# Kernel optimization log

Hardware: AMD Instinct MI355X
Metric: run time of the kernel (lower is better)

## Reference

```python
import jax, jax.numpy as jnp
import numpy as np

B, T, I, H = 1024, 2048, 12, 512


def setup_inputs() -> dict:
    key = jax.random.key(0)
    k1, k2, k3, k4 = jax.random.split(key, 4)
    s = 1.0 / np.sqrt(H)
    return {
        "history": jax.random.normal(k1, (B, T, I), dtype=jnp.float32),
        "w_ih": jax.random.normal(k2, (3 * H, I), dtype=jnp.float32) * s,
        "w_hh": jax.random.normal(k3, (3 * H, H), dtype=jnp.float32) * s,
        "w_out": jax.random.normal(k4, (2, H), dtype=jnp.float32) * s,
        "b_out": jnp.zeros((2,), dtype=jnp.float32),
    }


def reference(history, w_ih, w_hh, w_out, b_out):
    # GRUCell recurrence over T steps with per-step linear head (torch GRUCell math, bias=False)
    xs = jnp.transpose(history, (1, 0, 2))  # [T, B, I]
    h0 = jnp.zeros((history.shape[0], H), dtype=history.dtype)

    def step(h, x_t):
        gi = x_t @ w_ih.T            # [B, 3H]
        gh = h @ w_hh.T              # [B, 3H]
        i_r, i_z, i_n = jnp.split(gi, 3, axis=-1)
        h_r, h_z, h_n = jnp.split(gh, 3, axis=-1)
        r = jax.nn.sigmoid(i_r + h_r)
        z = jax.nn.sigmoid(i_z + h_z)
        n = jnp.tanh(i_n + r * h_n)
        h_new = (1.0 - z) * n + z * h
        logit = h_new @ w_out.T + b_out  # [B, 2]
        return h_new, logit

    h_final, logits = jax.lax.scan(step, h0, xs)
    return jnp.transpose(logits, (1, 0, 2)), h_final  # ([B, T, 2], [B, H])
```

## Files before the change

### kernel.cpp

```cpp
#include <hip/hip_runtime.h>
#include <stdint.h>


#define NB 256
#define NT 256
#define TB 1024
#define TT 2048
#define II 12
#define HH 512
#define NCL 32
#define ROWS 32

#define HTILE_B (ROWS * HH * 2)
#define HBUF_B  ((size_t)NCL * HTILE_B)
#define BAR_OFF ((size_t)2 * HBUF_B)
#define WS_USED (BAR_OFF + (size_t)NCL * 256)

#define LDSB (ROWS * 1024)

#define GAS __attribute__((address_space(1)))
#define LAS __attribute__((address_space(3)))

typedef _Float16 half8 __attribute__((ext_vector_type(8)));
typedef float    f32x4 __attribute__((ext_vector_type(4)));

static __device__ __forceinline__ float fast_sigmoid(float x) {
  float e = exp2f(-1.44269504f * x);
  return __builtin_amdgcn_rcpf(1.0f + e);
}
static __device__ __forceinline__ float fast_tanh(float x) {
  float e = exp2f(2.88539008f * x);
  return 1.0f - 2.0f * __builtin_amdgcn_rcpf(1.0f + e);
}

static __device__ __forceinline__ void wait_flags32(unsigned* f, unsigned tgt,
                                                    int* dead) {
  const int l = threadIdx.x & 63;
  long spin = 0;
  for (;;) {
    unsigned v = __hip_atomic_load(f + (l & 31), __ATOMIC_RELAXED,
                                   __HIP_MEMORY_SCOPE_AGENT);
    if (__all(v >= tgt)) break;
    if (++spin > (1L << 24)) { *dead = 1; break; }
  }
}

__global__ void __launch_bounds__(NT, 1)
gru_persistent(const float* __restrict__ hist,
               const float* __restrict__ w_ih,
               const float* __restrict__ w_hh,
               const float* __restrict__ w_out,
               const float* __restrict__ b_out,
               float* __restrict__ out,
               uint8_t* __restrict__ ws)
{
  extern __shared__ char smem[];
  char* ldsA = smem;
  const int bid = blockIdx.x;
  const int c   = bid & 31;
  const int g   = bid >> 5;
  const int tid = threadIdx.x;
  const int w   = tid >> 6;
  const int l   = tid & 63;
  const int l15 = l & 15;
  const int l4  = l >> 4;
  const int crb = c * ROWS;
  unsigned* loF = (unsigned*)(ws + BAR_OFF) + (size_t)c * 64;
  unsigned* hiF = loF + 32;
  const int myflag = g * 4 + w;

  const int col0 = g * 64 + w * 16;
  const int pcol = col0 + l15;

  half8 wr[16], wz[16], wn[16];
#pragma unroll
  for (int ks = 0; ks < 16; ++ks) {
    const size_t Rr = (size_t)(0 * HH + col0 + l15) * HH + ks * 32 + l4 * 8;
    const size_t Rz = (size_t)(1 * HH + col0 + l15) * HH + ks * 32 + l4 * 8;
    const size_t Rn = (size_t)(2 * HH + col0 + l15) * HH + ks * 32 + l4 * 8;
#pragma unroll
    for (int i = 0; i < 8; ++i) {
      wr[ks][i] = (_Float16)w_hh[Rr + i];
      wz[ks][i] = (_Float16)w_hh[Rz + i];
      wn[ks][i] = (_Float16)w_hh[Rn + i];
    }
  }

  half8 wih[3];
#pragma unroll
  for (int gt = 0; gt < 3; ++gt) {
    const int R = gt * HH + col0 + l15;
#pragma unroll
    for (int i = 0; i < 8; ++i) {
      const int k = l4 * 8 + i;
      wih[gt][i] = (_Float16)((k < II) ? w_ih[R * II + k] : 0.0f);
    }
  }

  const int jj   = myflag & 1;
  const int erow = myflag >> 1;
  float wor8[8];
#pragma unroll
  for (int i = 0; i < 8; ++i) wor8[i] = w_out[jj * HH + l * 8 + i];
  const float bo = b_out[jj];

  float hprev[2][4];
#pragma unroll
  for (int mt = 0; mt < 2; ++mt)
#pragma unroll
    for (int q = 0; q < 4; ++q) hprev[mt][q] = 0.0f;

  int deadlock = 0;

  f32x4 xn0[2], xn1[2];
#pragma unroll
  for (int mt = 0; mt < 2; ++mt) {
    xn0[mt] = (f32x4){0.f, 0.f, 0.f, 0.f};
    xn1[mt] = (f32x4){0.f, 0.f, 0.f, 0.f};
    const float* xp = hist + (size_t)(crb + mt * 16 + l15) * (TT * II);
    if (l4 == 0)      { xn0[mt] = *(const f32x4*)xp; xn1[mt] = *(const f32x4*)(xp + 4); }
    else if (l4 == 1) { xn0[mt] = *(const f32x4*)(xp + 8); }
  }
  asm volatile("s_waitcnt vmcnt(0)" ::: "memory");

  unsigned preLo = 0, preHi = 0;

  for (int t = 0; t < TT; ++t) {
    const uint8_t* hsrc = ws + ((t & 1) ? HBUF_B : 0) + (size_t)c * HTILE_B;
    uint8_t*       hdst = ws + ((t & 1) ? 0 : HBUF_B) + (size_t)c * HTILE_B;

    if (t > 0) {
      if (!__all(preLo >= (unsigned)t)) wait_flags32(loF, (unsigned)t, &deadlock);
    }
    __builtin_amdgcn_sched_barrier(0);

#pragma unroll
    for (int it = 0; it < 4; ++it)
      __builtin_amdgcn_global_load_lds(
          (const GAS uint32_t*)(hsrc + it * 4096 + tid * 16),
          (LAS uint32_t*)(ldsA + it * 4096 + tid * 16), 16, 0, 17);
    __builtin_amdgcn_sched_barrier(0);

    preHi = __hip_atomic_load(hiF + (l & 31), __ATOMIC_RELAXED,
                              __HIP_MEMORY_SCOPE_AGENT);
    __builtin_amdgcn_sched_barrier(0);
    half8 ax[2];
#pragma unroll
    for (int mt = 0; mt < 2; ++mt)
#pragma unroll
      for (int i = 0; i < 4; ++i) {
        ax[mt][i]     = (_Float16)xn0[mt][i];
        ax[mt][4 + i] = (_Float16)xn1[mt][i];
      }
    {
      const int tx = (t + 1 < TT) ? (t + 1) : 0;
#pragma unroll
      for (int mt = 0; mt < 2; ++mt) {
        const float* xp = hist + (size_t)(crb + mt * 16 + l15) * (TT * II) + (size_t)tx * II;
        if (l4 == 0)      { xn0[mt] = *(const f32x4*)xp; xn1[mt] = *(const f32x4*)(xp + 4); }
        else if (l4 == 1) { xn0[mt] = *(const f32x4*)(xp + 8); }
      }
    }
    __builtin_amdgcn_sched_barrier(0);

    asm volatile("s_waitcnt vmcnt(6)" ::: "memory");
    __builtin_amdgcn_sched_barrier(0);
    if (t > 0 && !__all(preHi >= (unsigned)t)) wait_flags32(hiF, (unsigned)t, &deadlock);
    __builtin_amdgcn_sched_barrier(0);

#pragma unroll
    for (int it = 0; it < 4; ++it)
      __builtin_amdgcn_global_load_lds(
          (const GAS uint32_t*)(hsrc + 16384 + it * 4096 + tid * 16),
          (LAS uint32_t*)(ldsA + 16384 + it * 4096 + tid * 16), 16, 0, 17);
    __builtin_amdgcn_sched_barrier(0);

    __builtin_amdgcn_s_barrier();
    __builtin_amdgcn_sched_barrier(0);

    f32x4 acc0 = (f32x4){0.f, 0.f, 0.f, 0.f};
    f32x4 acc1 = acc0, acc2 = acc0;
    f32x4 accin = __builtin_amdgcn_mfma_f32_16x16x32_f16(ax[0], wih[2],
                    (f32x4){0.f, 0.f, 0.f, 0.f}, 0, 0, 0);
    acc0 = __builtin_amdgcn_mfma_f32_16x16x32_f16(ax[0], wih[0], acc0, 0, 0, 0);
    acc1 = __builtin_amdgcn_mfma_f32_16x16x32_f16(ax[0], wih[1], acc1, 0, 0, 0);
#pragma unroll
    for (int ks = 0; ks < 16; ++ks) {
      const int ko = (ks * 64 + l4 * 16) ^ ((l15 & 7) << 4);
      half8 a = *(const half8*)(ldsA + l15 * 1024 + ko);
      acc0 = __builtin_amdgcn_mfma_f32_16x16x32_f16(a, wr[ks], acc0, 0, 0, 0);
      acc1 = __builtin_amdgcn_mfma_f32_16x16x32_f16(a, wz[ks], acc1, 0, 0, 0);
      acc2 = __builtin_amdgcn_mfma_f32_16x16x32_f16(a, wn[ks], acc2, 0, 0, 0);
    }

#pragma unroll
    for (int q = 0; q < 4; ++q) {
      const int m = l4 * 4 + q;
      const float r  = fast_sigmoid(acc0[q]);
      const float z  = fast_sigmoid(acc1[q]);
      const float n  = fast_tanh(accin[q] + r * acc2[q]);
      const float hn = (1.0f - z) * n + z * hprev[0][q];
      hprev[0][q] = hn;
      __hip_atomic_store(
          (unsigned short*)(hdst + m * 1024 + ((pcol * 2) ^ ((m & 7) << 4))),
          __builtin_bit_cast(unsigned short, (_Float16)hn),
          __ATOMIC_RELAXED, __HIP_MEMORY_SCOPE_AGENT);
    }

    if (t > 0) {
      float s = 0.0f;
      half8 hv = *(const half8*)(ldsA + erow * 1024 + ((l * 16) ^ ((erow & 7) << 4)));
#pragma unroll
      for (int i = 0; i < 8; ++i) s += (float)hv[i] * wor8[i];
#pragma unroll
      for (int off = 1; off < 64; off <<= 1) s += __shfl_xor(s, off);
      if (l == 0) out[((size_t)(crb + erow) * TT + (t - 1)) * 2 + jj] = s + bo;
    }
    __builtin_amdgcn_sched_barrier(0);

    asm volatile("s_waitcnt vmcnt(0)" ::: "memory");
    __builtin_amdgcn_sched_barrier(0);
    if (l == 0)
      __hip_atomic_store(loF + myflag, (unsigned)(t + 1), __ATOMIC_RELAXED,
                         __HIP_MEMORY_SCOPE_AGENT);

    __builtin_amdgcn_s_barrier();
    __builtin_amdgcn_sched_barrier(0);

    acc0 = (f32x4){0.f, 0.f, 0.f, 0.f};
    acc1 = acc0; acc2 = acc0;
    accin = __builtin_amdgcn_mfma_f32_16x16x32_f16(ax[1], wih[2],
              (f32x4){0.f, 0.f, 0.f, 0.f}, 0, 0, 0);
    acc0 = __builtin_amdgcn_mfma_f32_16x16x32_f16(ax[1], wih[0], acc0, 0, 0, 0);
    acc1 = __builtin_amdgcn_mfma_f32_16x16x32_f16(ax[1], wih[1], acc1, 0, 0, 0);
#pragma unroll
    for (int ks = 0; ks < 16; ++ks) {
      const int ko = (ks * 64 + l4 * 16) ^ ((l15 & 7) << 4);
      half8 a = *(const half8*)(ldsA + (16 + l15) * 1024 + ko);
      acc0 = __builtin_amdgcn_mfma_f32_16x16x32_f16(a, wr[ks], acc0, 0, 0, 0);
      acc1 = __builtin_amdgcn_mfma_f32_16x16x32_f16(a, wz[ks], acc1, 0, 0, 0);
      acc2 = __builtin_amdgcn_mfma_f32_16x16x32_f16(a, wn[ks], acc2, 0, 0, 0);
    }
#pragma unroll
    for (int q = 0; q < 4; ++q) {
      const int m = 16 + l4 * 4 + q;
      const float r  = fast_sigmoid(acc0[q]);
      const float z  = fast_sigmoid(acc1[q]);
      const float n  = fast_tanh(accin[q] + r * acc2[q]);
      const float hn = (1.0f - z) * n + z * hprev[1][q];
      hprev[1][q] = hn;
      __hip_atomic_store(
          (unsigned short*)(hdst + m * 1024 + ((pcol * 2) ^ ((m & 7) << 4))),
          __builtin_bit_cast(unsigned short, (_Float16)hn),
          __ATOMIC_RELAXED, __HIP_MEMORY_SCOPE_AGENT);
    }

    if (t > 0) {
      const int lrw = 16 + erow;
      float s = 0.0f;
      half8 hv = *(const half8*)(ldsA + lrw * 1024 + ((l * 16) ^ ((lrw & 7) << 4)));
#pragma unroll
      for (int i = 0; i < 8; ++i) s += (float)hv[i] * wor8[i];
#pragma unroll
      for (int off = 1; off < 64; off <<= 1) s += __shfl_xor(s, off);
      if (l == 0) out[((size_t)(crb + lrw) * TT + (t - 1)) * 2 + jj] = s + bo;
    }
    __builtin_amdgcn_sched_barrier(0);

    asm volatile("s_waitcnt vmcnt(0)" ::: "memory");
    __builtin_amdgcn_sched_barrier(0);
    if (l == 0)
      __hip_atomic_store(hiF + myflag, (unsigned)(t + 1), __ATOMIC_RELAXED,
                         __HIP_MEMORY_SCOPE_AGENT);
    preLo = __hip_atomic_load(loF + (l & 31), __ATOMIC_RELAXED,
                              __HIP_MEMORY_SCOPE_AGENT);
  }

  asm volatile("s_waitcnt vmcnt(0)" ::: "memory");
  wait_flags32(loF, (unsigned)TT, &deadlock);
  wait_flags32(hiF, (unsigned)TT, &deadlock);
  {
    const uint8_t* hsrc = ws + ((TT & 1) ? HBUF_B : 0) + (size_t)c * HTILE_B;
#pragma unroll
    for (int it = 0; it < 8; ++it)
      __builtin_amdgcn_global_load_lds(
          (const GAS uint32_t*)(hsrc + it * 4096 + tid * 16),
          (LAS uint32_t*)(ldsA + it * 4096 + tid * 16), 16, 0, 17);
    asm volatile("s_waitcnt vmcnt(0)" ::: "memory");
    __builtin_amdgcn_s_barrier();

#pragma unroll
    for (int half = 0; half < 2; ++half) {
      const int lrw = half * 16 + erow;
      float s = 0.0f;
      half8 hv = *(const half8*)(ldsA + lrw * 1024 + ((l * 16) ^ ((lrw & 7) << 4)));
#pragma unroll
      for (int i = 0; i < 8; ++i) s += (float)hv[i] * wor8[i];
#pragma unroll
      for (int off = 1; off < 64; off <<= 1) s += __shfl_xor(s, off);
      if (l == 0) out[((size_t)(crb + lrw) * TT + (TT - 1)) * 2 + jj] = s + bo;
    }
  }

#pragma unroll
  for (int mt = 0; mt < 2; ++mt)
#pragma unroll
    for (int q = 0; q < 4; ++q) {
      const int m = mt * 16 + l4 * 4 + q;
      out[(size_t)TB * TT * 2 + (size_t)(crb + m) * HH + pcol] = hprev[mt][q];
    }
}

extern "C" void kernel_launch(void* const* d_in, const int* in_sizes, int n_in,
                              void* d_out, int out_size, void* d_ws, size_t ws_size,
                              hipStream_t stream) {
  (void)in_sizes; (void)n_in; (void)out_size;
  if (ws_size < WS_USED) return;

  const float* hist  = (const float*)d_in[0];
  const float* w_ih  = (const float*)d_in[1];
  const float* w_hh  = (const float*)d_in[2];
  const float* w_out = (const float*)d_in[3];
  const float* b_out = (const float*)d_in[4];
  float* out = (float*)d_out;
  uint8_t* ws = (uint8_t*)d_ws;

  hipMemsetAsync(d_ws, 0, WS_USED, stream);

  void* args[] = {(void*)&hist, (void*)&w_ih, (void*)&w_hh, (void*)&w_out,
                  (void*)&b_out, (void*)&out, (void*)&ws};
  hipError_t e = hipLaunchCooperativeKernel((const void*)gru_persistent,
                                            dim3(NB), dim3(NT), args,
                                            (unsigned)LDSB, stream);
  if (e != hipSuccess) {
    gru_persistent<<<dim3(NB), dim3(NT), LDSB, stream>>>(
        hist, w_ih, w_hh, w_out, b_out, out, ws);
  }
}
```

Measured before the change: 9.109 ms.

## Merge split lo/hi step flags into one flag set and load full tile

```diff
diff --git a/kernel.cpp b/kernel.cpp
--- a/kernel.cpp
+++ b/kernel.cpp
@@ -14,7 +14,7 @@
 #define HTILE_B (ROWS * HH * 2)
 #define HBUF_B  ((size_t)NCL * HTILE_B)
 #define BAR_OFF ((size_t)2 * HBUF_B)
-#define WS_USED (BAR_OFF + (size_t)NCL * 256)
+#define WS_USED (BAR_OFF + (size_t)NCL * 128)
 
 #define LDSB (ROWS * 1024)
 
@@ -65,8 +65,7 @@
   const int l15 = l & 15;
   const int l4  = l >> 4;
   const int crb = c * ROWS;
-  unsigned* loF = (unsigned*)(ws + BAR_OFF) + (size_t)c * 64;
-  unsigned* hiF = loF + 32;
+  unsigned* F = (unsigned*)(ws + BAR_OFF) + (size_t)c * 32;
   const int myflag = g * 4 + w;
 
   const int col0 = g * 64 + w * 16;
@@ -121,29 +120,25 @@
     if (l4 == 0)      { xn0[mt] = *(const f32x4*)xp; xn1[mt] = *(const f32x4*)(xp + 4); }
     else if (l4 == 1) { xn0[mt] = *(const f32x4*)(xp + 8); }
   }
-  asm volatile("s_waitcnt vmcnt(0)" ::: "memory");
-
-  unsigned preLo = 0, preHi = 0;
+
+  unsigned preF = 0;
 
   for (int t = 0; t < TT; ++t) {
     const uint8_t* hsrc = ws + ((t & 1) ? HBUF_B : 0) + (size_t)c * HTILE_B;
     uint8_t*       hdst = ws + ((t & 1) ? 0 : HBUF_B) + (size_t)c * HTILE_B;
 
     if (t > 0) {
-      if (!__all(preLo >= (unsigned)t)) wait_flags32(loF, (unsigned)t, &deadlock);
-    }
-    __builtin_amdgcn_sched_barrier(0);
-
-#pragma unroll
-    for (int it = 0; it < 4; ++it)
+      if (!__all(preF >= (unsigned)t)) wait_flags32(F, (unsigned)t, &deadlock);
+    }
+    __builtin_amdgcn_sched_barrier(0);
+
+#pragma unroll
+    for (int it = 0; it < 8; ++it)
       __builtin_amdgcn_global_load_lds(
           (const GAS uint32_t*)(hsrc + it * 4096 + tid * 16),
           (LAS uint32_t*)(ldsA + it * 4096 + tid * 16), 16, 0, 17);
     __builtin_amdgcn_sched_barrier(0);
 
-    preHi = __hip_atomic_load(hiF + (l & 31), __ATOMIC_RELAXED,
-                              __HIP_MEMORY_SCOPE_AGENT);
-    __builtin_amdgcn_sched_barrier(0);
     half8 ax[2];
 #pragma unroll
     for (int mt = 0; mt < 2; ++mt)
@@ -152,29 +147,9 @@
         ax[mt][i]     = (_Float16)xn0[mt][i];
         ax[mt][4 + i] = (_Float16)xn1[mt][i];
       }
-    {
-      const int tx = (t + 1 < TT) ? (t + 1) : 0;
-#pragma unroll
-      for (int mt = 0; mt < 2; ++mt) {
-        const float* xp = hist + (size_t)(crb + mt * 16 + l15) * (TT * II) + (size_t)tx * II;
-        if (l4 == 0)      { xn0[mt] = *(const f32x4*)xp; xn1[mt] = *(const f32x4*)(xp + 4); }
-        else if (l4 == 1) { xn0[mt] = *(const f32x4*)(xp + 8); }
-      }
-    }
-    __builtin_amdgcn_sched_barrier(0);
-
-    asm volatile("s_waitcnt vmcnt(6)" ::: "memory");
-    __builtin_amdgcn_sched_barrier(0);
-    if (t > 0 && !__all(preHi >= (unsigned)t)) wait_flags32(hiF, (unsigned)t, &deadlock);
-    __builtin_amdgcn_sched_barrier(0);
-
-#pragma unroll
-    for (int it = 0; it < 4; ++it)
-      __builtin_amdgcn_global_load_lds(
-          (const GAS uint32_t*)(hsrc + 16384 + it * 4096 + tid * 16),
-          (LAS uint32_t*)(ldsA + 16384 + it * 4096 + tid * 16), 16, 0, 17);
-    __builtin_amdgcn_sched_barrier(0);
-
+    __builtin_amdgcn_sched_barrier(0);
+
+    asm volatile("s_waitcnt vmcnt(4)" ::: "memory");
     __builtin_amdgcn_s_barrier();
     __builtin_amdgcn_sched_barrier(0);
 
@@ -206,24 +181,9 @@
           __builtin_bit_cast(unsigned short, (_Float16)hn),
           __ATOMIC_RELAXED, __HIP_MEMORY_SCOPE_AGENT);
     }
-
-    if (t > 0) {
-      float s = 0.0f;
-      half8 hv = *(const half8*)(ldsA + erow * 1024 + ((l * 16) ^ ((erow & 7) << 4)));
-#pragma unroll
-      for (int i = 0; i < 8; ++i) s += (float)hv[i] * wor8[i];
-#pragma unroll
-      for (int off = 1; off < 64; off <<= 1) s += __shfl_xor(s, off);
-      if (l == 0) out[((size_t)(crb + erow) * TT + (t - 1)) * 2 + jj] = s + bo;
-    }
-    __builtin_amdgcn_sched_barrier(0);
-
-    asm volatile("s_waitcnt vmcnt(0)" ::: "memory");
-    __builtin_amdgcn_sched_barrier(0);
-    if (l == 0)
-      __hip_atomic_store(loF + myflag, (unsigned)(t + 1), __ATOMIC_RELAXED,
-                         __HIP_MEMORY_SCOPE_AGENT);
-
+    __builtin_amdgcn_sched_barrier(0);
+
+    asm volatile("s_waitcnt vmcnt(4)" ::: "memory");
     __builtin_amdgcn_s_barrier();
     __builtin_amdgcn_sched_barrier(0);
 
@@ -256,29 +216,42 @@
     }
 
     if (t > 0) {
-      const int lrw = 16 + erow;
-      float s = 0.0f;
-      half8 hv = *(const half8*)(ldsA + lrw * 1024 + ((l * 16) ^ ((lrw & 7) << 4)));
-#pragma unroll
-      for (int i = 0; i < 8; ++i) s += (float)hv[i] * wor8[i];
-#pragma unroll
-      for (int off = 1; off < 64; off <<= 1) s += __shfl_xor(s, off);
-      if (l == 0) out[((size_t)(crb + lrw) * TT + (t - 1)) * 2 + jj] = s + bo;
+#pragma unroll
+      for (int half = 0; half < 2; ++half) {
+        const int lrw = half * 16 + erow;
+        float s = 0.0f;
+        half8 hv = *(const half8*)(ldsA + lrw * 1024 + ((l * 16) ^ ((lrw & 7) << 4)));
+#pragma unroll
+        for (int i = 0; i < 8; ++i) s += (float)hv[i] * wor8[i];
+#pragma unroll
+        for (int off = 1; off < 64; off <<= 1) s += __shfl_xor(s, off);
+        if (l == 0) out[((size_t)(crb + lrw) * TT + (t - 1)) * 2 + jj] = s + bo;
+      }
     }
     __builtin_amdgcn_sched_barrier(0);
 
     asm volatile("s_waitcnt vmcnt(0)" ::: "memory");
     __builtin_amdgcn_sched_barrier(0);
     if (l == 0)
-      __hip_atomic_store(hiF + myflag, (unsigned)(t + 1), __ATOMIC_RELAXED,
+      __hip_atomic_store(F + myflag, (unsigned)(t + 1), __ATOMIC_RELAXED,
                          __HIP_MEMORY_SCOPE_AGENT);
-    preLo = __hip_atomic_load(loF + (l & 31), __ATOMIC_RELAXED,
-                              __HIP_MEMORY_SCOPE_AGENT);
+    preF = __hip_atomic_load(F + (l & 31), __ATOMIC_RELAXED,
+                             __HIP_MEMORY_SCOPE_AGENT);
+    __builtin_amdgcn_sched_barrier(0);
+    {
+      const int tx = (t + 1 < TT) ? (t + 1) : 0;
+#pragma unroll
+      for (int mt = 0; mt < 2; ++mt) {
+        const float* xp = hist + (size_t)(crb + mt * 16 + l15) * (TT * II) + (size_t)tx * II;
+        if (l4 == 0)      { xn0[mt] = *(const f32x4*)xp; xn1[mt] = *(const f32x4*)(xp + 4); }
+        else if (l4 == 1) { xn0[mt] = *(const f32x4*)(xp + 8); }
+      }
+    }
+    __builtin_amdgcn_sched_barrier(0);
   }
 
   asm volatile("s_waitcnt vmcnt(0)" ::: "memory");
-  wait_flags32(loF, (unsigned)TT, &deadlock);
-  wait_flags32(hiF, (unsigned)TT, &deadlock);
+  wait_flags32(F, (unsigned)TT, &deadlock);
   {
     const uint8_t* hsrc = ws + ((TT & 1) ? HBUF_B : 0) + (size_t)c * HTILE_B;
 #pragma unroll
```

After: 10.96 ms. +20.3%, slower.
